# Optimization experiments

Measured on AMD Instinct MI355X. Metric: run time of the kernel, lower is better.

## Reference

```python
import jax, jax.numpy as jnp
import numpy as np

KS = 3  # deformable kernel size

def conv2d(x, w, pad, stride=1):
    return jax.lax.conv_general_dilated(
        x, w, (stride, stride), [(pad, pad), (pad, pad)],
        dimension_numbers=('NCHW', 'OIHW', 'NCHW'))

def deform_conv(x, wp, bp, wc):
    # Faithful port of DeformConv2d(inc, outc, kernel_size=3, padding=1, stride=1)
    b, c, h, w = x.shape
    N = KS * KS
    offset = conv2d(x, wp, 1) + bp[None, :, None, None]  # [b, 2N, h, w]
    xpad = jnp.pad(x, ((0, 0), (0, 0), (1, 1), (1, 1)))
    Hp, Wp = h + 2, w + 2
    # p_n: kernel-relative offsets (x coords first, then y coords)
    rng = jnp.arange(-(KS - 1) // 2, (KS - 1) // 2 + 1, dtype=x.dtype)
    pnx, pny = jnp.meshgrid(rng, rng, indexing='ij')
    p_n = jnp.concatenate([pnx.reshape(-1), pny.reshape(-1)])  # [2N]
    # p_0: base sampling grid (1-indexed into padded map)
    p0x = jnp.broadcast_to(jnp.arange(1, h + 1, dtype=x.dtype)[:, None], (h, w))
    p0y = jnp.broadcast_to(jnp.arange(1, w + 1, dtype=x.dtype)[None, :], (h, w))
    p0 = jnp.concatenate([jnp.broadcast_to(p0x, (N, h, w)),
                          jnp.broadcast_to(p0y, (N, h, w))], 0)  # [2N,h,w]
    p = p0[None] + p_n[None, :, None, None] + offset  # [b,2N,h,w]
    p = jnp.transpose(p, (0, 2, 3, 1))  # [b,h,w,2N]
    qf = jax.lax.stop_gradient(jnp.floor(p))
    qltx = jnp.clip(qf[..., :N], 0, Hp - 1)
    qlty = jnp.clip(qf[..., N:], 0, Wp - 1)
    qrbx = jnp.clip(qf[..., :N] + 1, 0, Hp - 1)
    qrby = jnp.clip(qf[..., N:] + 1, 0, Wp - 1)
    px = jnp.clip(p[..., :N], 0, Hp - 1)
    py = jnp.clip(p[..., N:], 0, Wp - 1)
    g_lt = (1 + (qltx - px)) * (1 + (qlty - py))
    g_rb = (1 - (qrbx - px)) * (1 - (qrby - py))
    g_lb = (1 + (qltx - px)) * (1 - (qrby - py))
    g_rt = (1 - (qrbx - px)) * (1 + (qlty - py))
    xflat = xpad.reshape(b, c, Hp * Wp)
    def gather(qx, qy):
        idx = (qx.astype(jnp.int32) * Wp + qy.astype(jnp.int32)).reshape(b, 1, -1)
        idx = jnp.broadcast_to(idx, (b, c, idx.shape[-1]))
        return jnp.take_along_axis(xflat, idx, axis=2).reshape(b, c, h, w, N)
    xo = (g_lt[:, None] * gather(qltx, qlty) + g_rb[:, None] * gather(qrbx, qrby)
          + g_lb[:, None] * gather(qltx, qrby) + g_rt[:, None] * gather(qrbx, qlty))
    # rearrange 'b c h w (i j) -> b c (h i) (w j)'
    xo = xo.reshape(b, c, h, w, KS, KS).transpose(0, 1, 2, 4, 3, 5).reshape(b, c, h * KS, w * KS)
    return conv2d(xo, wc, 1, stride=KS)


def setup_inputs() -> dict:
    key = jax.random.key(0)
    B, C, H, W = 4, 64, 256, 256
    DIM, S0 = 64, 5
    ks = jax.random.split(key, 14)
    s = 0.02
    inp = {
        'x': jax.random.normal(ks[0], (B, C, H, W), jnp.float32),
        'wp_a': jax.random.normal(ks[1], (2 * KS * KS, C, 3, 3), jnp.float32) * s,
        'bp_a': jnp.zeros((2 * KS * KS,), jnp.float32),
        'wc_a': jax.random.normal(ks[2], (C, C, KS, KS), jnp.float32) * s,
        'w1_a': jax.random.normal(ks[3], (C, C, 1, 1), jnp.float32) * s,
        'b1_a': jax.random.normal(ks[4], (C,), jnp.float32) * s,
        'wp_p': jax.random.normal(ks[5], (2 * KS * KS, C, 3, 3), jnp.float32) * s,
        'bp_p': jnp.zeros((2 * KS * KS,), jnp.float32),
        'wc_p': jax.random.normal(ks[6], (C, C, KS, KS), jnp.float32) * s,
        'w1_p': jax.random.normal(ks[7], (C, C, 1, 1), jnp.float32) * s,
        'b1_p': jax.random.normal(ks[8], (C,), jnp.float32) * s,
        'w0': jax.random.normal(ks[9], (DIM, C, S0, S0), jnp.float32) * s,
        'b0': jax.random.normal(ks[10], (DIM,), jnp.float32) * s,
    }
    return inp


def reference(x, wp_a, bp_a, wc_a, w1_a, b1_a, wp_p, bp_p, wc_p, w1_p, b1_p, w0, b0):
    H, W = x.shape[2], x.shape[3]
    xf = jnp.fft.rfft2(x, axes=(2, 3))
    amp = jnp.abs(xf)
    pha = jnp.angle(xf)
    amp3 = deform_conv(amp, wp_a, bp_a, wc_a)
    amp1 = conv2d(amp, w1_a, 0) + b1_a[None, :, None, None]
    pha3 = deform_conv(pha, wp_p, bp_p, wc_p)
    pha1 = conv2d(pha, w1_p, 0) + b1_p[None, :, None, None]
    eps = 1e-08
    real_13 = amp1 * jnp.cos(pha3) + eps
    imag_31 = amp3 * jnp.sin(pha1) + eps
    real_31 = amp3 * jnp.cos(pha1) + eps
    imag_13 = amp1 * jnp.sin(pha3) + eps
    out_c = (real_13 + real_31) + 1j * (imag_31 + imag_13) + eps
    xr = jnp.abs(jnp.fft.irfft2(out_c, s=(H, W), axes=(2, 3)))
    s0 = w0.shape[2]
    return conv2d(xr, w0, s0 // 2) + b0[None, :, None, None]
```

## Files before the change

### kernel.cpp

```cpp
#include <hip/hip_runtime.h>
#include <math.h>

#define BB 4
#define CC 64
#define HH 256
#define WW 256
#define WF 129
#define NPIX (WF*HH)
#define NS ((size_t)BB*CC*NPIX)
#define TWOPI 6.283185307179586f

typedef __attribute__((ext_vector_type(8))) short short8v;
typedef __attribute__((ext_vector_type(4))) float float4v;
typedef __attribute__((ext_vector_type(16))) float float16v;

__device__ __forceinline__ float2 cmulf(float2 a, float2 b) {
    return make_float2(a.x*b.x - a.y*b.y, a.x*b.y + a.y*b.x);
}

template<int SIGN>
__device__ __forceinline__ float2 fft256_lds(const float2* __restrict__ xs,
                                             float2* __restrict__ ys,
                                             const float2* __restrict__ tw,
                                             const float2* __restrict__ tw16,
                                             int t) {
    int k1 = t & 15, n2 = t >> 4;
    float2 acc = make_float2(0.f, 0.f);
    #pragma unroll
    for (int n1 = 0; n1 < 16; ++n1) {
        float2 v = xs[n1*16 + n2];
        float2 w = tw16[(n1*k1) & 15];
        float ws = (SIGN < 0) ? -w.y : w.y;
        acc.x = fmaf(v.x, w.x, fmaf(-v.y, ws, acc.x));
        acc.y = fmaf(v.x, ws, fmaf( v.y, w.x, acc.y));
    }
    float2 w2 = tw[n2*k1];
    float w2s = (SIGN < 0) ? -w2.y : w2.y;
    ys[t] = cmulf(acc, make_float2(w2.x, w2s));
    __syncthreads();
    float2 acc2 = make_float2(0.f, 0.f);
    #pragma unroll
    for (int m2 = 0; m2 < 16; ++m2) {
        float2 v = ys[m2*16 + k1];
        float2 w = tw16[(m2*n2) & 15];
        float ws = (SIGN < 0) ? -w.y : w.y;
        acc2.x = fmaf(v.x, w.x, fmaf(-v.y, ws, acc2.x));
        acc2.y = fmaf(v.x, ws, fmaf( v.y, w.x, acc2.y));
    }
    return acc2;
}

template<int SIGN>
__device__ __forceinline__ float2 fft256_ip(float2* __restrict__ buf,
                                            const float2* __restrict__ tw,
                                            const float2* __restrict__ tw16,
                                            int t) {
    int k1 = t & 15, n2 = t >> 4;
    float2 acc = make_float2(0.f, 0.f);
    #pragma unroll
    for (int n1 = 0; n1 < 16; ++n1) {
        float2 v = buf[n1*16 + n2];
        float2 w = tw16[(n1*k1) & 15];
        float ws = (SIGN < 0) ? -w.y : w.y;
        acc.x = fmaf(v.x, w.x, fmaf(-v.y, ws, acc.x));
        acc.y = fmaf(v.x, ws, fmaf( v.y, w.x, acc.y));
    }
    float2 w2 = tw[n2*k1];
    float w2s = (SIGN < 0) ? -w2.y : w2.y;
    float2 mid = cmulf(acc, make_float2(w2.x, w2s));
    __syncthreads();
    buf[t] = mid;
    __syncthreads();
    float2 acc2 = make_float2(0.f, 0.f);
    #pragma unroll
    for (int m2 = 0; m2 < 16; ++m2) {
        float2 v = buf[m2*16 + k1];
        float2 w = tw16[(m2*n2) & 15];
        float ws = (SIGN < 0) ? -w.y : w.y;
        acc2.x = fmaf(v.x, w.x, fmaf(-v.y, ws, acc2.x));
        acc2.y = fmaf(v.x, ws, fmaf( v.y, w.x, acc2.y));
    }
    return acc2;
}

__global__ void k_tw(float2* __restrict__ twg) {
    int m = threadIdx.x;
    float s, c;
    sincosf((TWOPI/256.f) * (float)m, &s, &c);
    twg[m] = make_float2(c, s);
}

__global__ __launch_bounds__(256) void k_fft_rows(const float* __restrict__ x,
                                                  const float2* __restrict__ twg,
                                                  float* __restrict__ r1re,
                                                  float* __restrict__ r1im) {
    __shared__ float2 work[256];
    __shared__ float tileRe[16][132], tileIm[16][132];
    __shared__ float2 tw[256];
    __shared__ float2 tw16[16];
    int t = threadIdx.x;
    int bid = blockIdx.x;
    int yt = bid & 15;
    int bc = bid >> 4;
    int y0 = yt*16;
    tw[t] = twg[t];
    if (t < 16) tw16[t] = twg[t*16];
    const float* xb = x + (size_t)bc*HH*WW + (size_t)y0*WW;
    for (int r = 0; r < 16; ++r) {
        __syncthreads();
        work[t] = make_float2(xb[r*WW + t], 0.f);
        __syncthreads();
        float2 X = fft256_ip<-1>(work, tw, tw16, t);
        if (t < WF) { tileRe[r][t] = X.x; tileIm[r][t] = X.y; }
    }
    __syncthreads();
    if (t < WF) {
        size_t base = ((size_t)bc*WF + t)*HH + y0;
        #pragma unroll
        for (int g = 0; g < 4; ++g) {
            float4 vr = make_float4(tileRe[g*4][t], tileRe[g*4+1][t],
                                    tileRe[g*4+2][t], tileRe[g*4+3][t]);
            float4 vi = make_float4(tileIm[g*4][t], tileIm[g*4+1][t],
                                    tileIm[g*4+2][t], tileIm[g*4+3][t]);
            *(float4*)&r1re[base + g*4] = vr;
            *(float4*)&r1im[base + g*4] = vi;
        }
    }
}

__global__ __launch_bounds__(256) void k_fft_cols(const float* __restrict__ r1re,
                                                  const float* __restrict__ r1im,
                                                  const float2* __restrict__ twg,
                                                  float* __restrict__ amp,
                                                  float* __restrict__ pha) {
    __shared__ float2 xs[256], ys[256];
    __shared__ float2 tw[256];
    __shared__ float2 tw16[16];
    int t = threadIdx.x;
    int bid = blockIdx.x;
    int k = bid % WF;
    int bc = bid / WF;
    size_t base = ((size_t)bc*WF + k)*HH;
    tw[t] = twg[t];
    if (t < 16) tw16[t] = twg[t*16];
    xs[t] = make_float2(r1re[base + t], r1im[base + t]);
    __syncthreads();
    float2 X = fft256_lds<-1>(xs, ys, tw, tw16, t);
    amp[base + t] = sqrtf(X.x*X.x + X.y*X.y);
    pha[base + t] = atan2f(X.y, X.x);
}

__global__ __launch_bounds__(256) void k_pack(const float* __restrict__ src,
                                              float* __restrict__ dst) {
    __shared__ float tile[64][65];
    int tid = threadIdx.x;
    int bid = blockIdx.x;
    int it = bid & 3;
    int rest = bid >> 2;
    int k = rest % WF;
    int b = rest / WF;
    int i0 = it*64;
    int ii = tid & 63;
    int cg = tid >> 6;
    for (int rep = 0; rep < 16; ++rep) {
        int c = cg*16 + rep;
        tile[c][ii] = src[(size_t)(b*CC + c)*NPIX + (size_t)k*HH + i0 + ii];
    }
    __syncthreads();
    for (int rep = 0; rep < 16; ++rep) {
        int m = cg*16 + rep;
        dst[((size_t)(b*WF + k)*HH + i0 + m)*CC + ii] = tile[ii][m];
    }
}

__device__ __forceinline__ unsigned short bf16r(float f) {
    unsigned u = __float_as_uint(f);
    unsigned r = (u + 0x7FFFu + ((u >> 16) & 1u)) >> 16;
    return (unsigned short)r;
}
__device__ __forceinline__ float bf16f(unsigned short h) {
    return __uint_as_float(((unsigned)h) << 16);
}

__global__ void k_wct(const float* __restrict__ wc,
                      unsigned short* __restrict__ wh,
                      unsigned short* __restrict__ wl) {
    int idx = blockIdx.x*256 + threadIdx.x;
    if (idx < 64*576) {
        int k = idx % 576;
        int oc = idx / 576;
        int pos = k >> 6;
        int c = k & 63;
        float v = wc[((size_t)oc*64 + c)*9 + pos];
        unsigned short h = bf16r(v);
        wh[idx] = h;
        wl[idx] = bf16r(v - bf16f(h));
    }
}

__global__ void k_wsplit(const float* __restrict__ w0,
                         unsigned short* __restrict__ whT,
                         unsigned short* __restrict__ wlT) {
    int idx = blockIdx.x*256 + threadIdx.x;
    if (idx < 25*64*64) {
        int c = idx & 63;
        int t = idx >> 6;
        int oc = t & 63;
        int tap = t >> 6;
        float v = w0[((size_t)oc*CC + c)*25 + tap];
        unsigned short h = bf16r(v);
        float l = v - bf16f(h);
        whT[idx] = h;
        wlT[idx] = bf16r(l);
    }
}

__global__ void k_wpt(const float* __restrict__ wpa, const float* __restrict__ wpp,
                      float* __restrict__ wta, float* __restrict__ wtp) {
    int idx = blockIdx.x*256 + threadIdx.x;
    if (idx < 64*162) {
        int c = idx / 162;
        int r = idx - c*162;
        int oc = r / 9, pos = r - oc*9;
        size_t s = ((size_t)oc*CC + c)*9 + pos;
        wta[idx] = wpa[s];
        wtp[idx] = wpp[s];
    }
}

__global__ __launch_bounds__(256) void k_off2(const float* __restrict__ amp,
                                              const float* __restrict__ pha,
                                              const float* __restrict__ wptA,
                                              const float* __restrict__ wptP,
                                              const float* __restrict__ bpA,
                                              const float* __restrict__ bpP,
                                              float* __restrict__ offa,
                                              float* __restrict__ offp) {
    __shared__ float colb[2][3][260];
    int tid = threadIdx.x;
    int bid = blockIdx.x;
    int sel = (bid >= BB*WF) ? 1 : 0;
    int rb = sel ? bid - BB*WF : bid;
    int j = rb % WF;
    int b = rb / WF;
    const float* img = sel ? pha : amp;
    const float* wpt = sel ? wptP : wptA;
    const float* bp  = sel ? bpP  : bpA;
    float* off = sel ? offp : offa;

    const float* ib = img + (size_t)b*CC*NPIX + (size_t)j*HH;
    bool jm = (j > 0), jp = (j < WF-1);

    float acc[18];
    #pragma unroll
    for (int o = 0; o < 18; ++o) acc[o] = bp[o];

    if (tid < 12) {
        int bufi = tid & 1;
        int dj = (tid >> 1) % 3;
        int e = tid / 6;
        colb[bufi][dj][e ? 257 : 0] = 0.f;
    }
    {
        const float* cb = ib;
        colb[0][1][tid+1] = cb[tid];
        colb[0][0][tid+1] = jm ? cb[tid - HH] : 0.f;
        colb[0][2][tid+1] = jp ? cb[tid + HH] : 0.f;
    }
    __syncthreads();

    for (int c = 0; c < CC; ++c) {
        int cur = c & 1;
        if (c + 1 < CC) {
            const float* cb = ib + (size_t)(c+1)*NPIX;
            colb[cur^1][1][tid+1] = cb[tid];
            colb[cur^1][0][tid+1] = jm ? cb[tid - HH] : 0.f;
            colb[cur^1][2][tid+1] = jp ? cb[tid + HH] : 0.f;
        }
        float v[9];
        #pragma unroll
        for (int di = 0; di < 3; ++di)
            #pragma unroll
            for (int dj = 0; dj < 3; ++dj)
                v[di*3+dj] = colb[cur][dj][tid + di];
        const float* wc = wpt + c*162;
        #pragma unroll
        for (int o = 0; o < 18; ++o) {
            #pragma unroll
            for (int p = 0; p < 9; ++p)
                acc[o] = fmaf(wc[o*9+p], v[p], acc[o]);
        }
        __syncthreads();
    }

    size_t ob = ((size_t)(b*18)*WF + j)*HH + tid;
    #pragma unroll
    for (int o = 0; o < 18; ++o)
        off[ob + (size_t)o*WF*HH] = acc[o];
}

#define SPAD 328
__global__ __launch_bounds__(256) void k_deform(const float* __restrict__ imgc,
                                                const float* __restrict__ off,
                                                const unsigned short* __restrict__ wh,
                                                const unsigned short* __restrict__ wl,
                                                float* __restrict__ out) {
    __shared__ int   cidx[4][144];
    __shared__ float cwgt[4][144];
    __shared__ __align__(16) unsigned short Sh[16][SPAD];
    __shared__ __align__(16) unsigned short Sl[16][SPAD];
    int tid = threadIdx.x;
    int bid = blockIdx.x;
    int it = bid & 15;
    int rest = bid >> 4;
    int j = rest % WF;
    int b = rest / WF;
    int i0 = it * 16;

    if (tid < 144) {
        int pix = tid / 9;
        int pos = tid % 9;
        int ki = pos / 3, kj = pos % 3;
        int i = i0 + pix;
        int r = 3*i + ki - 1;
        int s = 3*j + kj - 1;
        float g[4] = {0.f,0.f,0.f,0.f};
        int ix[4] = {-1,-1,-1,-1};
        if (r >= 0 && s >= 0) {
            int hq = r/3, nx = r%3;
            int wq = s/3, ny = s%3;
            int n = nx*3 + ny;
            float ox = off[((size_t)(b*18 + n)*WF + wq)*HH + hq];
            float oy = off[((size_t)(b*18 + 9 + n)*WF + wq)*HH + hq];
            float pxf = (float)(hq + nx) + ox;
            float pyf = (float)(wq + ny) + oy;
            float qx = floorf(pxf), qy = floorf(pyf);
            float qltx = fminf(fmaxf(qx, 0.f), 257.f);
            float qlty = fminf(fmaxf(qy, 0.f), 130.f);
            float qrbx = fminf(fmaxf(qx + 1.f, 0.f), 257.f);
            float qrby = fminf(fmaxf(qy + 1.f, 0.f), 130.f);
            float pxc = fminf(fmaxf(pxf, 0.f), 257.f);
            float pyc = fminf(fmaxf(pyf, 0.f), 130.f);
            float glt = (1.f + (qltx - pxc)) * (1.f + (qlty - pyc));
            float grb = (1.f - (qrbx - pxc)) * (1.f - (qrby - pyc));
            float glb = (1.f + (qltx - pxc)) * (1.f - (qrby - pyc));
            float grt = (1.f - (qrbx - pxc)) * (1.f + (qlty - pyc));
            int ax0 = (int)qltx, ax1 = (int)qrbx;
            int ay0 = (int)qlty, ay1 = (int)qrby;
            int cx[4] = {ax0, ax1, ax0, ax1};
            int cy[4] = {ay0, ay1, ay1, ay0};
            g[0]=glt; g[1]=grb; g[2]=glb; g[3]=grt;
            #pragma unroll
            for (int q = 0; q < 4; ++q) {
                int a = cx[q], bq = cy[q];
                ix[q] = (a >= 1 && a <= 256 && bq >= 1 && bq <= 129)
                        ? ((bq-1)*HH + (a-1))*CC : -1;
            }
        }
        #pragma unroll
        for (int q = 0; q < 4; ++q) { cidx[q][tid] = ix[q]; cwgt[q][tid] = g[q]; }
    }
    __syncthreads();

    const float* cb = imgc + (size_t)b * (size_t)WF * HH * CC;
    int lane = tid & 63;
    int w = tid >> 6;
    int l15 = lane & 15;
    int l4 = lane >> 4;
    float4v acc = {0.f, 0.f, 0.f, 0.f};
    const unsigned short* wbh = wh + (size_t)(w*16 + l15)*576 + l4*8;
    const unsigned short* wbl = wl + (size_t)(w*16 + l15)*576 + l4*8;

    for (int t = tid; t < 4096; t += 256) {
        int c = t & 63;
        int s = t >> 6;
        int pix = s >> 2, pos = s & 3;
        int combo = pix*9 + pos;
        float sum = 0.f;
        #pragma unroll
        for (int q = 0; q < 4; ++q) {
            int ofs = cidx[q][combo];
            float v = (ofs >= 0) ? cb[(size_t)ofs + c] : 0.f;
            sum += cwgt[q][combo] * v;
        }
        unsigned short h = bf16r(sum);
        Sh[pix][pos*64 + c] = h;
        Sl[pix][pos*64 + c] = bf16r(sum - bf16f(h));
    }
    __syncthreads();
    #pragma unroll
    for (int k0 = 0; k0 < 256; k0 += 32) {
        short8v Ah = *(const short8v*)&wbh[k0];
        short8v Al = *(const short8v*)&wbl[k0];
        short8v Bh = *(const short8v*)&Sh[l15][k0 + l4*8];
        short8v Bl = *(const short8v*)&Sl[l15][k0 + l4*8];
        acc = __builtin_amdgcn_mfma_f32_16x16x32_bf16(Ah, Bh, acc, 0, 0, 0);
        acc = __builtin_amdgcn_mfma_f32_16x16x32_bf16(Ah, Bl, acc, 0, 0, 0);
        acc = __builtin_amdgcn_mfma_f32_16x16x32_bf16(Al, Bh, acc, 0, 0, 0);
    }
    __syncthreads();

    for (int t = tid; t < 5120; t += 256) {
        int c = t & 63;
        int s = t >> 6;
        int pix = s / 5, pp = s - pix*5;
        int combo = pix*9 + 4 + pp;
        float sum = 0.f;
        #pragma unroll
        for (int q = 0; q < 4; ++q) {
            int ofs = cidx[q][combo];
            float v = (ofs >= 0) ? cb[(size_t)ofs + c] : 0.f;
            sum += cwgt[q][combo] * v;
        }
        unsigned short h = bf16r(sum);
        Sh[pix][pp*64 + c] = h;
        Sl[pix][pp*64 + c] = bf16r(sum - bf16f(h));
    }
    __syncthreads();
    #pragma unroll
    for (int k0 = 0; k0 < 320; k0 += 32) {
        short8v Ah = *(const short8v*)&wbh[256 + k0];
        short8v Al = *(const short8v*)&wbl[256 + k0];
        short8v Bh = *(const short8v*)&Sh[l15][k0 + l4*8];
        short8v Bl = *(const short8v*)&Sl[l15][k0 + l4*8];
        acc = __builtin_amdgcn_mfma_f32_16x16x32_bf16(Ah, Bh, acc, 0, 0, 0);
        acc = __builtin_amdgcn_mfma_f32_16x16x32_bf16(Ah, Bl, acc, 0, 0, 0);
        acc = __builtin_amdgcn_mfma_f32_16x16x32_bf16(Al, Bh, acc, 0, 0, 0);
    }

    size_t ob = (size_t)b*CC*NPIX + (size_t)j*HH + i0;
    #pragma unroll
    for (int r = 0; r < 4; ++r) {
        int oc = w*16 + l4*4 + r;
        out[ob + (size_t)oc*NPIX + l15] = acc[r];
    }
}

__global__ __launch_bounds__(256) void k_combine(const float* __restrict__ ampc,
                                                 const float* __restrict__ phac,
                                                 float* __restrict__ a3,
                                                 float* __restrict__ p3,
                                                 const float* __restrict__ w1a,
                                                 const float* __restrict__ b1a,
                                                 const float* __restrict__ w1p,
                                                 const float* __restrict__ b1p) {
    __shared__ float la[64][65], lp[64][65];
    int tid = threadIdx.x;
    int bid = blockIdx.x;
    int quarter = bid & 3;
    int rest = bid >> 2;
    int j = rest % WF;
    int b = rest / WF;
    int i0 = quarter * 64;
    size_t gbase = ((size_t)(b*WF + j)*HH + i0) * CC;
    for (int rep = 0; rep < 16; ++rep) {
        int t = rep*256 + tid;
        int pix = t >> 6;
        int c = t & 63;
        la[c][pix] = ampc[gbase + t];
        lp[c][pix] = phac[gbase + t];
    }
    __syncthreads();
    int ii = tid & 63;
    int wv = tid >> 6;
    float acc_a[16], acc_p[16];
    #pragma unroll
    for (int q = 0; q < 16; ++q) { acc_a[q] = b1a[wv*16+q]; acc_p[q] = b1p[wv*16+q]; }
    for (int c = 0; c < CC; ++c) {
        float av = la[c][ii], pv = lp[c][ii];
        #pragma unroll
        for (int q = 0; q < 16; ++q) {
            acc_a[q] += w1a[(wv*16+q)*CC + c] * av;
            acc_p[q] += w1p[(wv*16+q)*CC + c] * pv;
        }
    }
    #pragma unroll
    for (int q = 0; q < 16; ++q) {
        int oc = wv*16 + q;
        size_t idx = (size_t)(b*CC + oc)*NPIX + (size_t)j*HH + i0 + ii;
        float a3v = a3[idx];
        float p3v = p3[idx];
        float s1, c1, s3, c3;
        sincosf(acc_p[q], &s1, &c1);
        sincosf(p3v, &s3, &c3);
        float re = acc_a[q]*c3 + a3v*c1 + 3e-8f;
        float im = a3v*s1 + acc_a[q]*s3 + 2e-8f;
        a3[idx] = re;
        p3[idx] = im;
    }
}

__global__ __launch_bounds__(256) void k_ifft_cols(const float* __restrict__ ocre,
                                                   const float* __restrict__ ocim,
                                                   const float2* __restrict__ twg,
                                                   float* __restrict__ r2re,
                                                   float* __restrict__ r2im) {
    __shared__ float2 xs[256], ys[256];
    __shared__ float2 tw[256];
    __shared__ float2 tw16[16];
    int t = threadIdx.x;
    int bid = blockIdx.x;
    int k = bid % WF;
    int bc = bid / WF;
    size_t base = ((size_t)bc*WF + k)*HH;
    tw[t] = twg[t];
    if (t < 16) tw16[t] = twg[t*16];
    xs[t] = make_float2(ocre[base + t], ocim[base + t]);
    __syncthreads();
    float2 X = fft256_lds<1>(xs, ys, tw, tw16, t);
    r2re[base + t] = X.x * (1.0f/256.0f);
    r2im[base + t] = X.y * (1.0f/256.0f);
}

__global__ __launch_bounds__(256) void k_irfft_rows(const float* __restrict__ r2re,
                                                    const float* __restrict__ r2im,
                                                    const float2* __restrict__ twg,
                                                    float* __restrict__ xr) {
    __shared__ float2 work[256];
    __shared__ float tileRe[16][132], tileIm[16][132];
    __shared__ float2 tw[256];
    __shared__ float2 tw16[16];
    int t = threadIdx.x;
    int bid = blockIdx.x;
    int yt = bid & 15;
    int bc = bid >> 4;
    int y0 = yt*16;
    tw[t] = twg[t];
    if (t < 16) tw16[t] = twg[t*16];
    if (t < WF) {
        size_t base = ((size_t)bc*WF + t)*HH + y0;
        #pragma unroll
        for (int g = 0; g < 4; ++g) {
            float4 vr = *(const float4*)&r2re[base + g*4];
            float4 vi = *(const float4*)&r2im[base + g*4];
            tileRe[g*4+0][t] = vr.x; tileIm[g*4+0][t] = vi.x;
            tileRe[g*4+1][t] = vr.y; tileIm[g*4+1][t] = vi.y;
            tileRe[g*4+2][t] = vr.z; tileIm[g*4+2][t] = vi.z;
            tileRe[g*4+3][t] = vr.w; tileIm[g*4+3][t] = vi.w;
        }
    }
    __syncthreads();
    float* xb = xr + (size_t)bc*HH*WW + (size_t)y0*WW;
    int src = (t < WF) ? t : 256 - t;
    float sg = (t < WF) ? 1.f : -1.f;
    for (int r = 0; r < 16; ++r) {
        work[t] = make_float2(tileRe[r][src], sg*tileIm[r][src]);
        __syncthreads();
        float2 X = fft256_ip<1>(work, tw, tw16, t);
        xb[r*WW + t] = fabsf(X.x * (1.0f/256.0f));
        __syncthreads();
    }
}

__global__ __launch_bounds__(256) void k_split(const float* __restrict__ xr,
                                               unsigned short* __restrict__ xh,
                                               unsigned short* __restrict__ xl) {
    __shared__ float tile[64][65];
    int tid = threadIdx.x;
    int bid = blockIdx.x;
    int q = bid & 3;
    int y = (bid >> 2) & 255;
    int b = bid >> 10;
    int x0 = q*64;
    int lane = tid & 63;
    int cg = tid >> 6;
    for (int rep = 0; rep < 16; ++rep) {
        int c = cg*16 + rep;
        tile[c][lane] = xr[(((size_t)(b*CC + c)*HH + y)*WW) + x0 + lane];
    }
    __syncthreads();
    int x = tid >> 2;
    int c0 = (tid & 3)*8;
    #pragma unroll
    for (int ch = 0; ch < 2; ++ch) {
        short8v hv, lv;
        #pragma unroll
        for (int j = 0; j < 8; ++j) {
            float v = tile[ch*32 + c0 + j][x];
            unsigned short h = bf16r(v);
            float l = v - bf16f(h);
            hv[j] = (short)h;
            lv[j] = (short)bf16r(l);
        }
        size_t ob = ((((size_t)(b*2 + ch)*HH + y)*WW) + x0 + x)*32 + c0;
        *(short8v*)&xh[ob] = hv;
        *(short8v*)&xl[ob] = lv;
    }
}

#define CLX 68
#define CPART 544
#define CPLANE 1088

__global__ __launch_bounds__(256) void k_conv5m(const unsigned short* __restrict__ xh,
                                                const unsigned short* __restrict__ xl,
                                                const unsigned short* __restrict__ whT,
                                                const unsigned short* __restrict__ wlT,
                                                const float* __restrict__ b0,
                                                float* __restrict__ out) {
    __shared__ __align__(16) unsigned short smem[2*CPLANE*8];
    int tid = threadIdx.x;
    int bid = blockIdx.x;
    int q = bid & 3;
    int yb = (bid >> 2) & 63;
    int b = bid >> 8;
    int x0 = q*64;
    int y0 = yb*4;
    int lane = tid & 63;
    int w = tid >> 6;
    int l31 = lane & 31;
    int l1  = lane >> 5;

    int goffb[5], loffs[5];
    bool ok[5], has[5];
    #pragma unroll
    for (int s = 0; s < 5; ++s) {
        int item = (s < 4) ? (s*256 + tid) : (1024 + tid);
        bool h = (s < 4) || (tid < 64);
        int part = (item >= CPART) ? 1 : 0;
        int rest = item - part*CPART;
        int row = rest / CLX;
        int xi = rest - row*CLX;
        int gy = y0 + row - 2;
        int gx = x0 + xi - 2;
        bool o = h && gy >= 0 && gy < HH && gx >= 0 && gx < WW;
        has[s] = h; ok[s] = o;
        goffb[s] = o ? ((gy*WW + gx)*32 + part*8) : 0;
        loffs[s] = (part*CPART + row*CLX + xi)*8;
    }

    float16v acc[2][2];
    #pragma unroll
    for (int o2 = 0; o2 < 2; ++o2) {
        float16v bi;
        #pragma unroll
        for (int r = 0; r < 16; ++r)
            bi[r] = b0[o2*32 + (r & 3) + 8*(r >> 2) + 4*l1];
        acc[o2][0] = bi;
        acc[o2][1] = bi;
    }

    short8v rh[5], rl[5];
    const short8v zero8 = {0,0,0,0,0,0,0,0};

#define PREFETCH(P) do { \
        size_t chb = ((size_t)(b*2 + ((P) >> 1)) << 16) * 32; \
        int phofs = ((P) & 1) * 16; \
        _Pragma("unroll") \
        for (int s = 0; s < 5; ++s) { \
            if (has[s]) { \
                rh[s] = *(const short8v*)&xh[chb + goffb[s] + phofs]; \
                rl[s] = *(const short8v*)&xl[chb + goffb[s] + phofs]; \
            } \
        } \
    } while (0)

#define WRITE() do { \
        _Pragma("unroll") \
        for (int s = 0; s < 5; ++s) { \
            if (has[s]) { \
                *(short8v*)&smem[loffs[s]]              = ok[s] ? rh[s] : zero8; \
                *(short8v*)&smem[CPLANE*8 + loffs[s]]   = ok[s] ? rl[s] : zero8; \
            } \
        } \
    } while (0)

#define COMPUTE(P) do { \
        _Pragma("unroll 5") \
        for (int tap = 0; tap < 25; ++tap) { \
            int dy = tap / 5, dx = tap - dy*5; \
            size_t wb = ((size_t)(tap*64 + l31))*64 + (P)*16 + l1*8; \
            short8v Ah0 = *(const short8v*)&whT[wb]; \
            short8v Al0 = *(const short8v*)&wlT[wb]; \
            short8v Ah1 = *(const short8v*)&whT[wb + 2048]; \
            short8v Al1 = *(const short8v*)&wlT[wb + 2048]; \
            int a0 = (l1*CPART + (w + dy)*CLX + l31 + dx)*8; \
            short8v Bh0 = *(const short8v*)&smem[a0]; \
            short8v Bl0 = *(const short8v*)&smem[CPLANE*8 + a0]; \
            short8v Bh1 = *(const short8v*)&smem[a0 + 256]; \
            short8v Bl1 = *(const short8v*)&smem[CPLANE*8 + a0 + 256]; \
            acc[0][0] = __builtin_amdgcn_mfma_f32_32x32x16_bf16(Ah0, Bh0, acc[0][0], 0,0,0); \
            acc[0][1] = __builtin_amdgcn_mfma_f32_32x32x16_bf16(Ah0, Bh1, acc[0][1], 0,0,0); \
            acc[1][0] = __builtin_amdgcn_mfma_f32_32x32x16_bf16(Ah1, Bh0, acc[1][0], 0,0,0); \
            acc[1][1] = __builtin_amdgcn_mfma_f32_32x32x16_bf16(Ah1, Bh1, acc[1][1], 0,0,0); \
            acc[0][0] = __builtin_amdgcn_mfma_f32_32x32x16_bf16(Ah0, Bl0, acc[0][0], 0,0,0); \
            acc[0][1] = __builtin_amdgcn_mfma_f32_32x32x16_bf16(Ah0, Bl1, acc[0][1], 0,0,0); \
            acc[1][0] = __builtin_amdgcn_mfma_f32_32x32x16_bf16(Ah1, Bl0, acc[1][0], 0,0,0); \
            acc[1][1] = __builtin_amdgcn_mfma_f32_32x32x16_bf16(Ah1, Bl1, acc[1][1], 0,0,0); \
            acc[0][0] = __builtin_amdgcn_mfma_f32_32x32x16_bf16(Al0, Bh0, acc[0][0], 0,0,0); \
            acc[0][1] = __builtin_amdgcn_mfma_f32_32x32x16_bf16(Al0, Bh1, acc[0][1], 0,0,0); \
            acc[1][0] = __builtin_amdgcn_mfma_f32_32x32x16_bf16(Al1, Bh0, acc[1][0], 0,0,0); \
            acc[1][1] = __builtin_amdgcn_mfma_f32_32x32x16_bf16(Al1, Bh1, acc[1][1], 0,0,0); \
        } \
    } while (0)

    PREFETCH(0);
    WRITE();
    __syncthreads();
    PREFETCH(1);
    COMPUTE(0);
    __syncthreads();
    WRITE();
    __syncthreads();
    PREFETCH(2);
    COMPUTE(1);
    __syncthreads();
    WRITE();
    __syncthreads();
    PREFETCH(3);
    COMPUTE(2);
    __syncthreads();
    WRITE();
    __syncthreads();
    COMPUTE(3);

#undef PREFETCH
#undef WRITE
#undef COMPUTE

    int y = y0 + w;
    #pragma unroll
    for (int o2 = 0; o2 < 2; ++o2) {
        #pragma unroll
        for (int p2 = 0; p2 < 2; ++p2) {
            #pragma unroll
            for (int r = 0; r < 16; ++r) {
                int oc = o2*32 + (r & 3) + 8*(r >> 2) + 4*l1;
                int x = x0 + p2*32 + l31;
                out[(((size_t)(b*CC + oc)*HH + y)*WW) + x] = acc[o2][p2][r];
            }
        }
    }
}

extern "C" void kernel_launch(void* const* d_in, const int* in_sizes, int n_in,
                              void* d_out, int out_size, void* d_ws, size_t ws_size,
                              hipStream_t stream) {
    const float* x    = (const float*)d_in[0];
    const float* wp_a = (const float*)d_in[1];
    const float* bp_a = (const float*)d_in[2];
    const float* wc_a = (const float*)d_in[3];
    const float* w1_a = (const float*)d_in[4];
    const float* b1_a = (const float*)d_in[5];
    const float* wp_p = (const float*)d_in[6];
    const float* bp_p = (const float*)d_in[7];
    const float* wc_p = (const float*)d_in[8];
    const float* w1_p = (const float*)d_in[9];
    const float* b1_p = (const float*)d_in[10];
    const float* w0   = (const float*)d_in[11];
    const float* b0   = (const float*)d_in[12];
    float* out = (float*)d_out;
    float* ws  = (float*)d_ws;

    float* R0 = ws;
    float* R1 = ws + 2*NS;
    float* R2 = ws + 4*NS;

    float* r1re = R0;
    float* r1im = R0 + NS;
    float* amp  = R1;
    float* pha  = R1 + NS;
    float* ampc = R0;
    float* phac = R0 + NS;
    size_t offsz = (size_t)BB*18*NPIX;
    float* offa = R2;
    float* offp = R2 + offsz;
    unsigned short* wsp = (unsigned short*)(R2 + 2*offsz);
    unsigned short* whA = wsp;
    unsigned short* wlA = wsp + 36864;
    unsigned short* whP = wsp + 2*36864;
    unsigned short* wlP = wsp + 3*36864;
    unsigned short* whT = wsp + 4*36864;
    unsigned short* wlT = whT + 25*64*64;
    float* wptA = (float*)(wlT + 25*64*64);
    float* wptP = wptA + 64*162;
    float2* twg = (float2*)(wptP + 64*162);
    float* A3   = R1;
    float* P3   = R1 + NS;
    float* r2re = R0;
    float* r2im = R0 + NS;
    float* xrp  = R1;
    unsigned short* xhp = (unsigned short*)R0;
    unsigned short* xlp = xhp + (size_t)BB*2*HH*WW*32;

    k_tw<<<1, 256, 0, stream>>>(twg);
    k_wct<<<144, 256, 0, stream>>>(wc_a, whA, wlA);
    k_wct<<<144, 256, 0, stream>>>(wc_p, whP, wlP);
    k_wsplit<<<400, 256, 0, stream>>>(w0, whT, wlT);
    k_wpt<<<41, 256, 0, stream>>>(wp_a, wp_p, wptA, wptP);
    k_fft_rows<<<BB*CC*16, 256, 0, stream>>>(x, twg, r1re, r1im);
    k_fft_cols<<<BB*CC*WF, 256, 0, stream>>>(r1re, r1im, twg, amp, pha);
    k_pack<<<BB*WF*4, 256, 0, stream>>>(amp, ampc);
    k_pack<<<BB*WF*4, 256, 0, stream>>>(pha, phac);
    k_off2<<<2*BB*WF, 256, 0, stream>>>(amp, pha, wptA, wptP, bp_a, bp_p, offa, offp);
    k_deform<<<BB*WF*16, 256, 0, stream>>>(ampc, offa, whA, wlA, A3);
    k_deform<<<BB*WF*16, 256, 0, stream>>>(phac, offp, whP, wlP, P3);
    k_combine<<<BB*WF*4, 256, 0, stream>>>(ampc, phac, A3, P3, w1_a, b1_a, w1_p, b1_p);
    k_ifft_cols<<<BB*CC*WF, 256, 0, stream>>>(A3, P3, twg, r2re, r2im);
    k_irfft_rows<<<BB*CC*16, 256, 0, stream>>>(r2re, r2im, twg, xrp);
    k_split<<<BB*HH*4, 256, 0, stream>>>(xrp, xhp, xlp);
    k_conv5m<<<BB*64*4, 256, 0, stream>>>(xhp, xlp, whT, wlT, b0, out);
}
```

Measured before the change: 1.464 ms.

## Stage conv5 input tiles via direct global-to-LDS loads with double buffering

Restructures the final 5x5 conv kernel to load input tiles straight into LDS with global_load_lds instead of going through registers, double-buffering the LDS tile so each phase's load overlaps the previous phase's compute. Out-of-bounds halo loads read from a zero page written by the twiddle kernel. It also software-pipelines the A/B fragment loads one tap ahead, remaps block indices to spread the batch across XCDs, and adds launch_bounds occupancy 2. The risks are higher register and LDS pressure from the doubled buffer, and that the LDS destination layout of global_load_lds must match the old loffs layout.

```diff
diff --git a/kernel.cpp b/kernel.cpp
--- a/kernel.cpp
+++ b/kernel.cpp
@@ -83,11 +83,12 @@
     return acc2;
 }
 
-__global__ void k_tw(float2* __restrict__ twg) {
+__global__ void k_tw(float2* __restrict__ twg, float* __restrict__ zp) {
     int m = threadIdx.x;
     float s, c;
     sincosf((TWOPI/256.f) * (float)m, &s, &c);
     twg[m] = make_float2(c, s);
+    zp[m] = 0.f;
 }
 
 __global__ __launch_bounds__(256) void k_fft_rows(const float* __restrict__ x,
@@ -588,19 +589,28 @@
     }
 }
 
+__device__ __forceinline__ void gload16(const void* g, void* l) {
+    __builtin_amdgcn_global_load_lds((const __attribute__((address_space(1))) void*)g,
+                                     (__attribute__((address_space(3))) void*)l,
+                                     16, 0, 0);
+}
+
 #define CLX 68
 #define CPART 544
 #define CPLANE 1088
-
-__global__ __launch_bounds__(256) void k_conv5m(const unsigned short* __restrict__ xh,
-                                                const unsigned short* __restrict__ xl,
-                                                const unsigned short* __restrict__ whT,
-                                                const unsigned short* __restrict__ wlT,
-                                                const float* __restrict__ b0,
-                                                float* __restrict__ out) {
-    __shared__ __align__(16) unsigned short smem[2*CPLANE*8];
+#define CBUF (2*CPLANE)
+
+__global__ __launch_bounds__(256, 2) void k_conv5m(const unsigned short* __restrict__ xh,
+                                                   const unsigned short* __restrict__ xl,
+                                                   const unsigned short* __restrict__ whT,
+                                                   const unsigned short* __restrict__ wlT,
+                                                   const float* __restrict__ b0,
+                                                   const float* __restrict__ zpage,
+                                                   float* __restrict__ out) {
+    __shared__ __align__(16) unsigned short smem[2*CBUF*8];
     int tid = threadIdx.x;
-    int bid = blockIdx.x;
+    int bid0 = blockIdx.x;
+    int bid = (bid0 & 7)*128 + (bid0 >> 3);
     int q = bid & 3;
     int yb = (bid >> 2) & 63;
     int b = bid >> 8;
@@ -610,9 +620,11 @@
     int w = tid >> 6;
     int l31 = lane & 31;
     int l1  = lane >> 5;
-
-    int goffb[5], loffs[5];
+    const unsigned short* zp = (const unsigned short*)zpage;
+
+    int goffb[5];
     bool ok[5], has[5];
+    int ldsu[5];
     #pragma unroll
     for (int s = 0; s < 5; ++s) {
         int item = (s < 4) ? (s*256 + tid) : (1024 + tid);
@@ -626,7 +638,7 @@
         bool o = h && gy >= 0 && gy < HH && gx >= 0 && gx < WW;
         has[s] = h; ok[s] = o;
         goffb[s] = o ? ((gy*WW + gx)*32 + part*8) : 0;
-        loffs[s] = (part*CPART + row*CLX + xi)*8;
+        ldsu[s] = ((s < 4) ? (s*256 + w*64) : (1024 + w*64)) * 8;
     }
 
     float16v acc[2][2];
@@ -640,82 +652,84 @@
         acc[o2][1] = bi;
     }
 
-    short8v rh[5], rl[5];
-    const short8v zero8 = {0,0,0,0,0,0,0,0};
-
-#define PREFETCH(P) do { \
+#define STAGE(P, BUF) do { \
         size_t chb = ((size_t)(b*2 + ((P) >> 1)) << 16) * 32; \
         int phofs = ((P) & 1) * 16; \
+        unsigned short* dbase = smem + (BUF)*CBUF*8; \
         _Pragma("unroll") \
         for (int s = 0; s < 5; ++s) { \
             if (has[s]) { \
-                rh[s] = *(const short8v*)&xh[chb + goffb[s] + phofs]; \
-                rl[s] = *(const short8v*)&xl[chb + goffb[s] + phofs]; \
+                const unsigned short* sh_ = ok[s] ? &xh[chb + goffb[s] + phofs] : zp; \
+                const unsigned short* sl_ = ok[s] ? &xl[chb + goffb[s] + phofs] : zp; \
+                gload16(sh_, dbase + ldsu[s]); \
+                gload16(sl_, dbase + CPLANE*8 + ldsu[s]); \
             } \
         } \
     } while (0)
 
-#define WRITE() do { \
-        _Pragma("unroll") \
-        for (int s = 0; s < 5; ++s) { \
-            if (has[s]) { \
-                *(short8v*)&smem[loffs[s]]              = ok[s] ? rh[s] : zero8; \
-                *(short8v*)&smem[CPLANE*8 + loffs[s]]   = ok[s] ? rl[s] : zero8; \
+#define LOADA(TAP, P, A) do { \
+        size_t wb = ((size_t)((TAP)*64 + l31))*64 + (P)*16 + l1*8; \
+        A[0] = *(const short8v*)&whT[wb]; \
+        A[1] = *(const short8v*)&whT[wb + 2048]; \
+        A[2] = *(const short8v*)&wlT[wb]; \
+        A[3] = *(const short8v*)&wlT[wb + 2048]; \
+    } while (0)
+
+#define LOADB(TAP, BUF, Bv) do { \
+        int dy_ = (TAP) / 5, dx_ = (TAP) - dy_*5; \
+        int a0 = (BUF)*CBUF*8 + (l1*CPART + (w + dy_)*CLX + l31 + dx_)*8; \
+        Bv[0] = *(const short8v*)&smem[a0]; \
+        Bv[1] = *(const short8v*)&smem[a0 + 256]; \
+        Bv[2] = *(const short8v*)&smem[CPLANE*8 + a0]; \
+        Bv[3] = *(const short8v*)&smem[CPLANE*8 + a0 + 256]; \
+    } while (0)
+
+#define MFMAS(A, Bv) do { \
+        acc[0][0] = __builtin_amdgcn_mfma_f32_32x32x16_bf16(A[0], Bv[0], acc[0][0], 0,0,0); \
+        acc[0][1] = __builtin_amdgcn_mfma_f32_32x32x16_bf16(A[0], Bv[1], acc[0][1], 0,0,0); \
+        acc[1][0] = __builtin_amdgcn_mfma_f32_32x32x16_bf16(A[1], Bv[0], acc[1][0], 0,0,0); \
+        acc[1][1] = __builtin_amdgcn_mfma_f32_32x32x16_bf16(A[1], Bv[1], acc[1][1], 0,0,0); \
+        acc[0][0] = __builtin_amdgcn_mfma_f32_32x32x16_bf16(A[0], Bv[2], acc[0][0], 0,0,0); \
+        acc[0][1] = __builtin_amdgcn_mfma_f32_32x32x16_bf16(A[0], Bv[3], acc[0][1], 0,0,0); \
+        acc[1][0] = __builtin_amdgcn_mfma_f32_32x32x16_bf16(A[1], Bv[2], acc[1][0], 0,0,0); \
+        acc[1][1] = __builtin_amdgcn_mfma_f32_32x32x16_bf16(A[1], Bv[3], acc[1][1], 0,0,0); \
+        acc[0][0] = __builtin_amdgcn_mfma_f32_32x32x16_bf16(A[2], Bv[0], acc[0][0], 0,0,0); \
+        acc[0][1] = __builtin_amdgcn_mfma_f32_32x32x16_bf16(A[2], Bv[1], acc[0][1], 0,0,0); \
+        acc[1][0] = __builtin_amdgcn_mfma_f32_32x32x16_bf16(A[3], Bv[0], acc[1][0], 0,0,0); \
+        acc[1][1] = __builtin_amdgcn_mfma_f32_32x32x16_bf16(A[3], Bv[1], acc[1][1], 0,0,0); \
+    } while (0)
+
+#define COMPUTE(P, BUF) do { \
+        short8v Acur[4], Bcur[4], Anxt[4], Bnxt[4]; \
+        LOADA(0, P, Acur); LOADB(0, BUF, Bcur); \
+        _Pragma("unroll 5") \
+        for (int tap = 0; tap < 25; ++tap) { \
+            if (tap < 24) { LOADA(tap+1, P, Anxt); LOADB(tap+1, BUF, Bnxt); } \
+            MFMAS(Acur, Bcur); \
+            if (tap < 24) { \
+                Acur[0]=Anxt[0]; Acur[1]=Anxt[1]; Acur[2]=Anxt[2]; Acur[3]=Anxt[3]; \
+                Bcur[0]=Bnxt[0]; Bcur[1]=Bnxt[1]; Bcur[2]=Bnxt[2]; Bcur[3]=Bnxt[3]; \
             } \
         } \
     } while (0)
 
-#define COMPUTE(P) do { \
-        _Pragma("unroll 5") \
-        for (int tap = 0; tap < 25; ++tap) { \
-            int dy = tap / 5, dx = tap - dy*5; \
-            size_t wb = ((size_t)(tap*64 + l31))*64 + (P)*16 + l1*8; \
-            short8v Ah0 = *(const short8v*)&whT[wb]; \
-            short8v Al0 = *(const short8v*)&wlT[wb]; \
-            short8v Ah1 = *(const short8v*)&whT[wb + 2048]; \
-            short8v Al1 = *(const short8v*)&wlT[wb + 2048]; \
-            int a0 = (l1*CPART + (w + dy)*CLX + l31 + dx)*8; \
-            short8v Bh0 = *(const short8v*)&smem[a0]; \
-            short8v Bl0 = *(const short8v*)&smem[CPLANE*8 + a0]; \
-            short8v Bh1 = *(const short8v*)&smem[a0 + 256]; \
-            short8v Bl1 = *(const short8v*)&smem[CPLANE*8 + a0 + 256]; \
-            acc[0][0] = __builtin_amdgcn_mfma_f32_32x32x16_bf16(Ah0, Bh0, acc[0][0], 0,0,0); \
-            acc[0][1] = __builtin_amdgcn_mfma_f32_32x32x16_bf16(Ah0, Bh1, acc[0][1], 0,0,0); \
-            acc[1][0] = __builtin_amdgcn_mfma_f32_32x32x16_bf16(Ah1, Bh0, acc[1][0], 0,0,0); \
-            acc[1][1] = __builtin_amdgcn_mfma_f32_32x32x16_bf16(Ah1, Bh1, acc[1][1], 0,0,0); \
-            acc[0][0] = __builtin_amdgcn_mfma_f32_32x32x16_bf16(Ah0, Bl0, acc[0][0], 0,0,0); \
-            acc[0][1] = __builtin_amdgcn_mfma_f32_32x32x16_bf16(Ah0, Bl1, acc[0][1], 0,0,0); \
-            acc[1][0] = __builtin_amdgcn_mfma_f32_32x32x16_bf16(Ah1, Bl0, acc[1][0], 0,0,0); \
-            acc[1][1] = __builtin_amdgcn_mfma_f32_32x32x16_bf16(Ah1, Bl1, acc[1][1], 0,0,0); \
-            acc[0][0] = __builtin_amdgcn_mfma_f32_32x32x16_bf16(Al0, Bh0, acc[0][0], 0,0,0); \
-            acc[0][1] = __builtin_amdgcn_mfma_f32_32x32x16_bf16(Al0, Bh1, acc[0][1], 0,0,0); \
-            acc[1][0] = __builtin_amdgcn_mfma_f32_32x32x16_bf16(Al1, Bh0, acc[1][0], 0,0,0); \
-            acc[1][1] = __builtin_amdgcn_mfma_f32_32x32x16_bf16(Al1, Bh1, acc[1][1], 0,0,0); \
-        } \
-    } while (0)
-
-    PREFETCH(0);
-    WRITE();
-    __syncthreads();
-    PREFETCH(1);
-    COMPUTE(0);
-    __syncthreads();
-    WRITE();
-    __syncthreads();
-    PREFETCH(2);
-    COMPUTE(1);
-    __syncthreads();
-    WRITE();
-    __syncthreads();
-    PREFETCH(3);
-    COMPUTE(2);
-    __syncthreads();
-    WRITE();
-    __syncthreads();
-    COMPUTE(3);
-
-#undef PREFETCH
-#undef WRITE
+    STAGE(0, 0);
+    __syncthreads();
+    STAGE(1, 1);
+    COMPUTE(0, 0);
+    __syncthreads();
+    STAGE(2, 0);
+    COMPUTE(1, 1);
+    __syncthreads();
+    STAGE(3, 1);
+    COMPUTE(2, 0);
+    __syncthreads();
+    COMPUTE(3, 1);
+
+#undef STAGE
+#undef LOADA
+#undef LOADB
+#undef MFMAS
 #undef COMPUTE
 
     int y = y0 + w;
@@ -775,6 +789,7 @@
     float* wptA = (float*)(wlT + 25*64*64);
     float* wptP = wptA + 64*162;
     float2* twg = (float2*)(wptP + 64*162);
+    float* zpage = (float*)(twg + 256);
     float* A3   = R1;
     float* P3   = R1 + NS;
     float* r2re = R0;
@@ -783,7 +798,7 @@
     unsigned short* xhp = (unsigned short*)R0;
     unsigned short* xlp = xhp + (size_t)BB*2*HH*WW*32;
 
-    k_tw<<<1, 256, 0, stream>>>(twg);
+    k_tw<<<1, 256, 0, stream>>>(twg, zpage);
     k_wct<<<144, 256, 0, stream>>>(wc_a, whA, wlA);
     k_wct<<<144, 256, 0, stream>>>(wc_p, whP, wlP);
     k_wsplit<<<400, 256, 0, stream>>>(w0, whT, wlT);
@@ -799,5 +814,5 @@
     k_ifft_cols<<<BB*CC*WF, 256, 0, stream>>>(A3, P3, twg, r2re, r2im);
     k_irfft_rows<<<BB*CC*16, 256, 0, stream>>>(r2re, r2im, twg, xrp);
     k_split<<<BB*HH*4, 256, 0, stream>>>(xrp, xhp, xlp);
-    k_conv5m<<<BB*64*4, 256, 0, stream>>>(xhp, xlp, whT, wlT, b0, out);
-}
+    k_conv5m<<<BB*64*4, 256, 0, stream>>>(xhp, xlp, whT, wlT, b0, zpage, out);
+}
```

Measured after the change: 1.453 ms. About the same (-0.7%).
